# Kernel optimization log

Hardware: AMD Instinct MI355X
Metric: run time of the kernel (lower is better)

Reference implementation:

```python
import jax, jax.numpy as jnp
import numpy as np

# --- MLA config (DeepSeek-V3 style, scaled) ---
HIDDEN = 4096
N_HEADS = 32
Q_LORA = 1536
KV_LORA = 512
ROPE_D = 64
NOPE_D = 128
V_D = 128
Q_HEAD_D = NOPE_D + ROPE_D  # 192
EPS = 1e-6
SCALING = Q_HEAD_D ** (-0.5)
ROPE_THETA = 10000.0
B, S = 1, 2048


def rms_norm(x, w):
    var = jnp.mean(jnp.square(x.astype(jnp.float32)), axis=-1, keepdims=True)
    return (x * jax.lax.rsqrt(var + EPS)).astype(x.dtype) * w


def rotate_half(x):
    x1, x2 = jnp.split(x, 2, axis=-1)
    return jnp.concatenate([-x2, x1], axis=-1)


def apply_rope(x, cos, sin):
    # x: [B, H, S, ROPE_D]; cos/sin: [B, S, ROPE_D] -> unsqueeze head dim
    c = cos[:, None, :, :]
    s = sin[:, None, :, :]
    return x * c + rotate_half(x) * s


def setup_inputs() -> dict:
    key = jax.random.key(0)
    ks = jax.random.split(key, 8)
    hidden_states = jax.random.normal(ks[0], (B, S, HIDDEN), dtype=jnp.float32)
    # real RoPE tables
    inv_freq = 1.0 / (ROPE_THETA ** (np.arange(0, ROPE_D, 2, dtype=np.float32) / ROPE_D))
    t = np.arange(S, dtype=np.float32)
    freqs = np.outer(t, inv_freq)                      # [S, ROPE_D/2]
    emb = np.concatenate([freqs, freqs], axis=-1)      # [S, ROPE_D]
    cos = jnp.asarray(np.cos(emb))[None].repeat(B, 0)  # [B, S, ROPE_D]
    sin = jnp.asarray(np.sin(emb))[None].repeat(B, 0)
    scale = lambda fan_in: 1.0 / np.sqrt(fan_in)
    w_q_a = jax.random.normal(ks[1], (Q_LORA, HIDDEN), dtype=jnp.float32) * scale(HIDDEN)
    q_a_ln_w = jnp.ones((Q_LORA,), dtype=jnp.float32)
    w_q_b = jax.random.normal(ks[2], (N_HEADS * Q_HEAD_D, Q_LORA), dtype=jnp.float32) * scale(Q_LORA)
    w_kv_a = jax.random.normal(ks[3], (KV_LORA + ROPE_D, HIDDEN), dtype=jnp.float32) * scale(HIDDEN)
    kv_a_ln_w = jnp.ones((KV_LORA,), dtype=jnp.float32)
    w_kv_b = jax.random.normal(ks[4], (N_HEADS * (NOPE_D + V_D), KV_LORA), dtype=jnp.float32) * scale(KV_LORA)
    w_o = jax.random.normal(ks[5], (HIDDEN, N_HEADS * V_D), dtype=jnp.float32) * scale(N_HEADS * V_D)
    return {
        'hidden_states': hidden_states, 'cos': cos, 'sin': sin,
        'w_q_a': w_q_a, 'q_a_ln_w': q_a_ln_w, 'w_q_b': w_q_b,
        'w_kv_a': w_kv_a, 'kv_a_ln_w': kv_a_ln_w, 'w_kv_b': w_kv_b, 'w_o': w_o,
    }


def reference(hidden_states, cos, sin, w_q_a, q_a_ln_w, w_q_b, w_kv_a, kv_a_ln_w, w_kv_b, w_o):
    b, s, _ = hidden_states.shape
    # --- Q path: low-rank down + RMSNorm + up ---
    q_lat = rms_norm(hidden_states @ w_q_a.T, q_a_ln_w)              # [B,S,Q_LORA]
    q = (q_lat @ w_q_b.T).reshape(b, s, N_HEADS, Q_HEAD_D)
    q = q.transpose(0, 2, 1, 3)                                       # [B,H,S,Q_HEAD_D]
    q_nope, q_rot = q[..., :NOPE_D], q[..., NOPE_D:]                  # (note: source names swapped)
    # --- KV path: shared compressed latent + single rotary key ---
    ckv = hidden_states @ w_kv_a.T                                    # [B,S,KV_LORA+ROPE_D]
    k_lat, k_rot = ckv[..., :KV_LORA], ckv[..., KV_LORA:]
    kv = (rms_norm(k_lat, kv_a_ln_w) @ w_kv_b.T).reshape(b, s, N_HEADS, NOPE_D + V_D)
    kv = kv.transpose(0, 2, 1, 3)                                     # [B,H,S,NOPE_D+V_D]
    k_nope, v = kv[..., :NOPE_D], kv[..., NOPE_D:]
    k_rot = k_rot.reshape(b, 1, s, ROPE_D)                            # single rotary key head
    # --- partial RoPE on rotary slices ---
    q_rot = apply_rope(q_rot, cos, sin)
    k_rot = apply_rope(k_rot, cos, sin)
    k_rot = jnp.broadcast_to(k_rot, (b, N_HEADS, s, ROPE_D))
    query = jnp.concatenate([q_rot, q_nope], axis=-1)                 # [B,H,S,192]
    key = jnp.concatenate([k_rot, k_nope], axis=-1)                   # [B,H,S,192]
    # --- eager causal attention ---
    scores = jnp.einsum('bhqd,bhkd->bhqk', query, key) * SCALING
    causal = jnp.tril(jnp.ones((s, s), dtype=bool))
    scores = jnp.where(causal[None, None], scores, jnp.finfo(scores.dtype).min)
    probs = jax.nn.softmax(scores, axis=-1)
    attn = jnp.einsum('bhqk,bhkd->bhqd', probs, v)                    # [B,H,S,V_D]
    attn = attn.transpose(0, 2, 1, 3).reshape(b, s, N_HEADS * V_D)
    return attn @ w_o.T                                               # [B,S,HIDDEN]
```

## Files before the change

### kernel.cpp

```cpp
#include <hip/hip_runtime.h>

typedef unsigned short u16;
typedef u16 u16x4 __attribute__((ext_vector_type(4)));
typedef u16 u16x8 __attribute__((ext_vector_type(8)));
typedef float f32x4 __attribute__((ext_vector_type(4)));
typedef __bf16 bf16x8 __attribute__((ext_vector_type(8)));

#define S_LEN 2048
#define HIDDEN_D 4096
#define NHEADS 32
#define QLORA 1536
#define KVLORA 512
#define ROPED 64
#define NOPED 128
#define VDIM 128
#define QHD 192
#define SCALING_F 0.07216878364870323f

__device__ __forceinline__ u16 f2bf(float x) {
  union { float f; unsigned u; } v; v.f = x;
  unsigned r = v.u + 0x7fffu + ((v.u >> 16) & 1u);
  return (u16)(r >> 16);
}
__device__ __forceinline__ float bf2f(u16 x) {
  union { unsigned u; float f; } v; v.u = ((unsigned)x) << 16; return v.f;
}

__device__ __forceinline__ f32x4 mfma_bf16(u16x8 a, u16x8 b, f32x4 c) {
  return __builtin_amdgcn_mfma_f32_16x16x32_bf16(
      __builtin_bit_cast(bf16x8, a), __builtin_bit_cast(bf16x8, b), c, 0, 0, 0);
}

__global__ __launch_bounds__(256) void cvt_kernel(const float* __restrict__ in,
                                                  u16* __restrict__ out, int n4) {
  int i = blockIdx.x * 256 + threadIdx.x;
  if (i >= n4) return;
  f32x4 v = ((const f32x4*)in)[i];
  u16x4 o;
  o[0] = f2bf(v[0]); o[1] = f2bf(v[1]); o[2] = f2bf(v[2]); o[3] = f2bf(v[3]);
  ((u16x4*)out)[i] = o;
}


#define GEMM_PROLOGUE()                                                        \
  __shared__ u16 sA[2][128 * 64];                                              \
  __shared__ u16 sB[2][128 * 64];                                              \
  const int tid = threadIdx.x;                                                 \
  const int wid = tid >> 6, lane = tid & 63;                                   \
  const int lr = lane & 15, lg = lane >> 4;                                    \
  const int nbn = (N + 127) >> 7;                                              \
  const int bx = blockIdx.x % nbn, by = blockIdx.x / nbn;                      \
  const int bm = by << 7, bn = bx << 7;                                        \
  const int wm = (wid >> 1) << 6, wn = (wid & 1) << 6;                         \
  const int kbase = blockIdx.y * Ks;                                           \
  f32x4 acc[4][4] = {};                                                        \
  u16x8 areg[4], breg[4];                                                      \
  auto loadA = [&](int k0) {                                                   \
    _Pragma("unroll")                                                          \
    for (int i = 0; i < 4; ++i) {                                              \
      int chunk = i * 256 + tid;                                               \
      int row = chunk >> 3, c8 = chunk & 7;                                    \
      int gr = bm + row; if (gr >= M) gr = M - 1;                              \
      areg[i] = *(const u16x8*)(A + (size_t)gr * lda + k0 + (c8 << 3));        \
    }                                                                          \
  };                                                                           \
  auto loadB = [&](int k0) {                                                   \
    _Pragma("unroll")                                                          \
    for (int i = 0; i < 4; ++i) {                                              \
      int chunk = i * 256 + tid;                                               \
      int n = chunk >> 3, c8 = chunk & 7;                                      \
      int gn = bn + n; if (gn >= N) gn = N - 1;                                \
      breg[i] = *(const u16x8*)(B + (size_t)gn * ldb + k0 + (c8 << 3));        \
    }                                                                          \
  };                                                                           \
  auto writeAB = [&](int buf) {                                                \
    _Pragma("unroll")                                                          \
    for (int i = 0; i < 4; ++i) {                                              \
      *(u16x8*)&sA[buf][(i * 256 + tid) * 8] = areg[i];                        \
      *(u16x8*)&sB[buf][(i * 256 + tid) * 8] = breg[i];                        \
    }                                                                          \
  };                                                                           \
  auto compute = [&](int buf) {                                                \
    const u16* pa = sA[buf];                                                   \
    const u16* pb = sB[buf];                                                   \
    _Pragma("unroll")                                                          \
    for (int ks = 0; ks < 2; ++ks) {                                           \
      const int kof = ks * 32 + lg * 8;                                        \
      u16x8 av[4], bv[4];                                                      \
      _Pragma("unroll")                                                        \
      for (int m = 0; m < 4; ++m) av[m] = *(const u16x8*)&pa[(wm + m * 16 + lr) * 64 + kof]; \
      _Pragma("unroll")                                                        \
      for (int n = 0; n < 4; ++n) bv[n] = *(const u16x8*)&pb[(wn + n * 16 + lr) * 64 + kof]; \
      _Pragma("unroll")                                                        \
      for (int m = 0; m < 4; ++m)                                              \
        _Pragma("unroll")                                                      \
        for (int n = 0; n < 4; ++n)                                            \
          acc[m][n] = mfma_bf16(av[m], bv[n], acc[m][n]);                      \
    }                                                                          \
  };                                                                           \
  const int nk = Ks >> 6;                                                      \
  loadA(kbase); loadB(kbase);                                                  \
  writeAB(0);                                                                  \
  __syncthreads();                                                             \
  for (int t = 0; t < nk; ++t) {                                               \
    const int cur = t & 1;                                                     \
    if (t + 1 < nk) { loadA(kbase + ((t + 1) << 6)); loadB(kbase + ((t + 1) << 6)); } \
    compute(cur);                                                              \
    if (t + 1 < nk) { writeAB(cur ^ 1); }                                      \
    __syncthreads();                                                           \
  }

__global__ __launch_bounds__(256, 2) void gemm_ff(
    const u16* __restrict__ A, const u16* __restrict__ B, float* __restrict__ C,
    int M, int N, int Ks, int lda, int ldb, int ldc)
{
  C += (size_t)blockIdx.y * M * ldc;
  GEMM_PROLOGUE()
#pragma unroll
  for (int m = 0; m < 4; ++m) {
    const int row0 = bm + wm + m * 16 + (lg << 2);
#pragma unroll
    for (int n = 0; n < 4; ++n) {
      const int col = bn + wn + n * 16 + lr;
      if (col < N) {
#pragma unroll
        for (int r = 0; r < 4; ++r)
          C[(size_t)(row0 + r) * ldc + col] = acc[m][n][r];
      }
    }
  }
}

__global__ __launch_bounds__(256, 2) void gemm_fb(
    const u16* __restrict__ A, const u16* __restrict__ B, u16* __restrict__ C,
    int M, int N, int Ks, int lda, int ldb, int ldc)
{
  GEMM_PROLOGUE()
#pragma unroll
  for (int m = 0; m < 4; ++m) {
    const int row0 = bm + wm + m * 16 + (lg << 2);
#pragma unroll
    for (int n = 0; n < 4; ++n) {
      const int col = bn + wn + n * 16 + lr;
#pragma unroll
      for (int r = 0; r < 4; ++r)
        C[(size_t)(row0 + r) * ldc + col] = f2bf(acc[m][n][r]);
    }
  }
}

__global__ __launch_bounds__(256, 2) void gemm_kvb(
    const u16* __restrict__ A, const u16* __restrict__ B,
    u16* __restrict__ Knope, u16* __restrict__ Vt,
    int M, int N, int Ks, int lda, int ldb)
{
  GEMM_PROLOGUE()
#pragma unroll
  for (int m = 0; m < 4; ++m) {
    const int row0 = bm + wm + m * 16 + (lg << 2);
#pragma unroll
    for (int n = 0; n < 4; ++n) {
      const int col = bn + wn + n * 16 + lr;
      const int h = col >> 8, c = col & 255;
      if (c < 128) {
#pragma unroll
        for (int r = 0; r < 4; ++r)
          Knope[((size_t)h * 2048 + row0 + r) * 128 + c] = f2bf(acc[m][n][r]);
      } else {
        u16x4 v;
        v[0] = f2bf(acc[m][n][0]); v[1] = f2bf(acc[m][n][1]);
        v[2] = f2bf(acc[m][n][2]); v[3] = f2bf(acc[m][n][3]);
        *(u16x4*)&Vt[((size_t)h * 128 + (c - 128)) * 2048 + row0] = v;
      }
    }
  }
}

__global__ __launch_bounds__(256) void rms_kernel(const float* __restrict__ X,
                                                  const float* __restrict__ w,
                                                  u16* __restrict__ out, int D,
                                                  int nparts, size_t pstride) {
  const int row = blockIdx.x;
  const float* x = X + (size_t)row * D;
  __shared__ float sb[4];
  float ss = 0.f;
  for (int i = threadIdx.x * 4; i < D; i += 1024) {
    f32x4 v = *(const f32x4*)&x[i];
    for (int pp = 1; pp < nparts; ++pp) {
      f32x4 v2 = *(const f32x4*)&x[pp * pstride + i];
      v[0] += v2[0]; v[1] += v2[1]; v[2] += v2[2]; v[3] += v2[3];
    }
    ss += v[0] * v[0] + v[1] * v[1] + v[2] * v[2] + v[3] * v[3];
  }
#pragma unroll
  for (int off = 32; off >= 1; off >>= 1) ss += __shfl_xor(ss, off, 64);
  if ((threadIdx.x & 63) == 0) sb[threadIdx.x >> 6] = ss;
  __syncthreads();
  const float inv = rsqrtf((sb[0] + sb[1] + sb[2] + sb[3]) / (float)D + 1e-6f);
  u16* o = out + (size_t)row * D;
  for (int i = threadIdx.x * 4; i < D; i += 1024) {
    f32x4 v = *(const f32x4*)&x[i];
    for (int pp = 1; pp < nparts; ++pp) {
      f32x4 v2 = *(const f32x4*)&x[pp * pstride + i];
      v[0] += v2[0]; v[1] += v2[1]; v[2] += v2[2]; v[3] += v2[3];
    }
    f32x4 wv = *(const f32x4*)&w[i];
    u16x4 u;
    u[0] = f2bf(v[0] * inv * wv[0]); u[1] = f2bf(v[1] * inv * wv[1]);
    u[2] = f2bf(v[2] * inv * wv[2]); u[3] = f2bf(v[3] * inv * wv[3]);
    *(u16x4*)&o[i] = u;
  }
}

__global__ __launch_bounds__(256) void ckv_epi_kernel(const float* __restrict__ ckv,
    const float* __restrict__ w, const float* __restrict__ cosp, const float* __restrict__ sinp,
    u16* __restrict__ klatn, u16* __restrict__ krot, int nparts, size_t pstride) {
  const int s = blockIdx.x;
  const float* x = ckv + (size_t)s * 576;
  __shared__ float sb[4];
  const int i2 = threadIdx.x * 2;
  float a = 0.f, b = 0.f;
  for (int pp = 0; pp < nparts; ++pp) {
    a += x[pp * pstride + i2];
    b += x[pp * pstride + i2 + 1];
  }
  float ss = a * a + b * b;
#pragma unroll
  for (int off = 32; off >= 1; off >>= 1) ss += __shfl_xor(ss, off, 64);
  if ((threadIdx.x & 63) == 0) sb[threadIdx.x >> 6] = ss;
  __syncthreads();
  const float inv = rsqrtf((sb[0] + sb[1] + sb[2] + sb[3]) / 512.0f + 1e-6f);
  klatn[(size_t)s * 512 + i2]     = f2bf(a * inv * w[i2]);
  klatn[(size_t)s * 512 + i2 + 1] = f2bf(b * inv * w[i2 + 1]);
  if (threadIdx.x < 64) {
    const int d = threadIdx.x;
    float xr = 0.f, rrabs = 0.f;
    for (int pp = 0; pp < nparts; ++pp) {
      xr += x[pp * pstride + 512 + d];
      rrabs += x[pp * pstride + 512 + ((d < 32) ? (d + 32) : (d - 32))];
    }
    const float rr = (d < 32) ? -rrabs : rrabs;
    krot[(size_t)s * 64 + d] = f2bf(xr * cosp[s * 64 + d] + rr * sinp[s * 64 + d]);
  }
}

__global__ __launch_bounds__(256) void q_epi_kernel(const u16* __restrict__ q_raw,
    const float* __restrict__ cosp, const float* __restrict__ sinp, u16* __restrict__ Qb) {
  const int s = blockIdx.x;
  const u16* x = q_raw + (size_t)s * 6144;
  for (int idx = threadIdx.x; idx < 6144; idx += 256) {
    const int h = idx / 192, d = idx - h * 192;
    float v;
    if (d < 64) {
      const float xr = bf2f(x[h * 192 + 128 + d]);
      const float rr = (d < 32) ? -bf2f(x[h * 192 + 160 + d]) : bf2f(x[h * 192 + 96 + d]);
      v = xr * cosp[s * 64 + d] + rr * sinp[s * 64 + d];
    } else {
      v = bf2f(x[h * 192 + d - 64]);
    }
    Qb[((size_t)h * 2048 + s) * QHD + d] = f2bf(v * SCALING_F);
  }
}

__global__ __launch_bounds__(256, 2) void flash_kernel(
    const u16* __restrict__ Qb, const u16* __restrict__ Krot,
    const u16* __restrict__ Knope, const u16* __restrict__ Vt,
    u16* __restrict__ attnb)
{
  const int h = blockIdx.x & 31, qt = blockIdx.x >> 5;
  const int q0 = qt << 7;
  __shared__ u16 sK[64][QHD];
  __shared__ u16 sV[VDIM][64];
  __shared__ u16 sP[4][32][64];
  const int tid = threadIdx.x;
  const int wid = tid >> 6, lane = tid & 63;
  const int lr = lane & 15, lg = lane >> 4;

  u16x8 qf[2][6];
#pragma unroll
  for (int m = 0; m < 2; ++m) {
    const int row = q0 + wid * 32 + m * 16 + lr;
#pragma unroll
    for (int kk = 0; kk < 6; ++kk)
      qf[m][kk] = *(const u16x8*)&Qb[((size_t)h * 2048 + row) * QHD + kk * 32 + lg * 8];
  }

  f32x4 acc[2][8] = {};
  float mx[2][4], ls[2][4];
#pragma unroll
  for (int m = 0; m < 2; ++m)
#pragma unroll
    for (int r = 0; r < 4; ++r) { mx[m][r] = -1e30f; ls[m][r] = 0.f; }

  const int nkv = q0 + 128;
  u16x8 kreg[6], vreg[4];

  auto loadKV = [&](int kv0) {
#pragma unroll
    for (int i = 0; i < 6; ++i) {
      const int chunk = i * 256 + tid;
      const int row = chunk / 24, cc = chunk % 24;
      const u16* src = (cc < 8)
          ? &Krot[(size_t)(kv0 + row) * 64 + cc * 8]
          : &Knope[((size_t)h * 2048 + kv0 + row) * 128 + (cc - 8) * 8];
      kreg[i] = *(const u16x8*)src;
    }
#pragma unroll
    for (int i = 0; i < 4; ++i) {
      const int chunk = i * 256 + tid;
      const int d = chunk >> 3, c = chunk & 7;
      vreg[i] = *(const u16x8*)&Vt[((size_t)h * VDIM + d) * 2048 + kv0 + c * 8];
    }
  };

  loadKV(0);
  for (int kv0 = 0; kv0 < nkv; kv0 += 64) {
    __syncthreads();
    u16* kbase = &sK[0][0];
#pragma unroll
    for (int i = 0; i < 6; ++i) *(u16x8*)&kbase[(size_t)(i * 256 + tid) * 8] = kreg[i];
    u16* vbase = &sV[0][0];
#pragma unroll
    for (int i = 0; i < 4; ++i) *(u16x8*)&vbase[(size_t)(i * 256 + tid) * 8] = vreg[i];
    __syncthreads();
    if (kv0 + 64 < nkv) loadKV(kv0 + 64);

    f32x4 sc[2][4] = {};
#pragma unroll
    for (int kk = 0; kk < 6; ++kk) {
      u16x8 bfr[4];
#pragma unroll
      for (int n = 0; n < 4; ++n) bfr[n] = *(const u16x8*)&sK[n * 16 + lr][kk * 32 + lg * 8];
#pragma unroll
      for (int m = 0; m < 2; ++m)
#pragma unroll
        for (int n = 0; n < 4; ++n)
          sc[m][n] = mfma_bf16(qf[m][kk], bfr[n], sc[m][n]);
    }

    if (kv0 + 63 > q0 + wid * 32) {
#pragma unroll
      for (int m = 0; m < 2; ++m)
#pragma unroll
        for (int n = 0; n < 4; ++n) {
          const int kv = kv0 + n * 16 + lr;
#pragma unroll
          for (int r = 0; r < 4; ++r) {
            const int rowq = q0 + wid * 32 + m * 16 + lg * 4 + r;
            if (kv > rowq) sc[m][n][r] = -1e30f;
          }
        }
    }

#pragma unroll
    for (int m = 0; m < 2; ++m) {
      float rs[4];
#pragma unroll
      for (int r = 0; r < 4; ++r) {
        float v = fmaxf(fmaxf(sc[m][0][r], sc[m][1][r]), fmaxf(sc[m][2][r], sc[m][3][r]));
#pragma unroll
        for (int off = 1; off < 16; off <<= 1) v = fmaxf(v, __shfl_xor(v, off, 64));
        const float mnew = fmaxf(mx[m][r], v);
        const float alpha = __expf(mx[m][r] - mnew);
        mx[m][r] = mnew;
        ls[m][r] *= alpha;
#pragma unroll
        for (int df = 0; df < 8; ++df) acc[m][df][r] *= alpha;
        rs[r] = 0.f;
      }
#pragma unroll
      for (int n = 0; n < 4; ++n)
#pragma unroll
        for (int r = 0; r < 4; ++r) {
          const float p = __expf(sc[m][n][r] - mx[m][r]);
          rs[r] += p;
          sP[wid][m * 16 + lg * 4 + r][n * 16 + lr] = f2bf(p);
        }
#pragma unroll
      for (int r = 0; r < 4; ++r) {
        float v = rs[r];
#pragma unroll
        for (int off = 1; off < 16; off <<= 1) v += __shfl_xor(v, off, 64);
        ls[m][r] += v;
      }
    }

#pragma unroll
    for (int ks = 0; ks < 2; ++ks) {
      u16x8 pf0 = *(const u16x8*)&sP[wid][lr][ks * 32 + lg * 8];
      u16x8 pf1 = *(const u16x8*)&sP[wid][16 + lr][ks * 32 + lg * 8];
#pragma unroll
      for (int df = 0; df < 8; ++df) {
        u16x8 vf = *(const u16x8*)&sV[df * 16 + lr][ks * 32 + lg * 8];
        acc[0][df] = mfma_bf16(pf0, vf, acc[0][df]);
        acc[1][df] = mfma_bf16(pf1, vf, acc[1][df]);
      }
    }
  }

#pragma unroll
  for (int m = 0; m < 2; ++m)
#pragma unroll
    for (int df = 0; df < 8; ++df) {
      const int col = h * 128 + df * 16 + lr;
#pragma unroll
      for (int r = 0; r < 4; ++r) {
        const int row = q0 + wid * 32 + m * 16 + lg * 4 + r;
        attnb[(size_t)row * 4096 + col] = f2bf(acc[m][df][r] / ls[m][r]);
      }
    }
}

extern "C" void kernel_launch(void* const* d_in, const int* in_sizes, int n_in,
                              void* d_out, int out_size, void* d_ws, size_t ws_size,
                              hipStream_t stream) {
  (void)in_sizes; (void)n_in; (void)out_size; (void)ws_size;
  const float* hidden  = (const float*)d_in[0];
  const float* cosp    = (const float*)d_in[1];
  const float* sinp    = (const float*)d_in[2];
  const float* w_q_a   = (const float*)d_in[3];
  const float* q_a_ln  = (const float*)d_in[4];
  const float* w_q_b   = (const float*)d_in[5];
  const float* w_kv_a  = (const float*)d_in[6];
  const float* kv_a_ln = (const float*)d_in[7];
  const float* w_kv_b  = (const float*)d_in[8];
  const float* w_o     = (const float*)d_in[9];
  float* out = (float*)d_out;

  char* p = (char*)d_ws;
  auto alloc = [&](size_t bytes) { char* r = p; p += (bytes + 255) & ~(size_t)255; return r; };
  u16* Hb     = (u16*)alloc((size_t)S_LEN * HIDDEN_D * 2);
  u16* qlatn  = (u16*)alloc((size_t)S_LEN * QLORA * 2);
  u16* klatn  = (u16*)alloc((size_t)S_LEN * KVLORA * 2);
  u16* krot   = (u16*)alloc((size_t)S_LEN * ROPED * 2);
  u16* Qb     = (u16*)alloc((size_t)NHEADS * S_LEN * QHD * 2);
  u16* Knope  = (u16*)alloc((size_t)NHEADS * S_LEN * NOPED * 2);
  u16* Vt     = (u16*)alloc((size_t)NHEADS * VDIM * S_LEN * 2);
  u16* attnb  = (u16*)alloc((size_t)S_LEN * 4096 * 2);
  u16* Wqa    = (u16*)alloc((size_t)QLORA * HIDDEN_D * 2);
  u16* Wqb    = (u16*)alloc((size_t)6144 * QLORA * 2);
  u16* Wkva   = (u16*)alloc((size_t)576 * HIDDEN_D * 2);
  u16* Wkvb   = (u16*)alloc((size_t)8192 * KVLORA * 2);
  u16* Wo     = (u16*)alloc((size_t)HIDDEN_D * 4096 * 2);
  u16* qraw16 = (u16*)alloc((size_t)S_LEN * 6144 * 2);
  float* qa_part  = (float*)alloc((size_t)2 * S_LEN * QLORA * 4);
  float* kva_part = (float*)alloc((size_t)4 * S_LEN * 576 * 4);

  cvt_kernel<<<(S_LEN * HIDDEN_D / 4 + 255) / 256, 256, 0, stream>>>(hidden, Hb, S_LEN * HIDDEN_D / 4);
  cvt_kernel<<<(QLORA * HIDDEN_D / 4 + 255) / 256, 256, 0, stream>>>(w_q_a, Wqa, QLORA * HIDDEN_D / 4);
  cvt_kernel<<<(6144 * QLORA / 4 + 255) / 256, 256, 0, stream>>>(w_q_b, Wqb, 6144 * QLORA / 4);
  cvt_kernel<<<(576 * HIDDEN_D / 4 + 255) / 256, 256, 0, stream>>>(w_kv_a, Wkva, 576 * HIDDEN_D / 4);
  cvt_kernel<<<(8192 * KVLORA / 4 + 255) / 256, 256, 0, stream>>>(w_kv_b, Wkvb, 8192 * KVLORA / 4);
  cvt_kernel<<<(HIDDEN_D * 4096 / 4 + 255) / 256, 256, 0, stream>>>(w_o, Wo, HIDDEN_D * 4096 / 4);

  gemm_ff<<<dim3(16 * 12, 2), 256, 0, stream>>>(Hb, Wqa, qa_part, 2048, 1536, 2048, 4096, 4096, 1536);
  gemm_ff<<<dim3(16 * 5, 4), 256, 0, stream>>>(Hb, Wkva, kva_part, 2048, 576, 1024, 4096, 4096, 576);
  rms_kernel<<<2048, 256, 0, stream>>>(qa_part, q_a_ln, qlatn, 1536, 2, (size_t)S_LEN * QLORA);
  ckv_epi_kernel<<<2048, 256, 0, stream>>>(kva_part, kv_a_ln, cosp, sinp, klatn, krot, 4, (size_t)S_LEN * 576);
  gemm_fb<<<dim3(16 * 48, 1), 256, 0, stream>>>(qlatn, Wqb, qraw16, 2048, 6144, 1536, 1536, 1536, 6144);
  q_epi_kernel<<<2048, 256, 0, stream>>>(qraw16, cosp, sinp, Qb);
  gemm_kvb<<<dim3(16 * 64, 1), 256, 0, stream>>>(klatn, Wkvb, Knope, Vt, 2048, 8192, 512, 512, 512);
  flash_kernel<<<512, 256, 0, stream>>>(Qb, krot, Knope, Vt, attnb);
  gemm_ff<<<dim3(16 * 32, 1), 256, 0, stream>>>(attnb, Wo, out, 2048, 4096, 4096, 4096, 4096, 4096);
}
```

Baseline: 604.7 us.

## Load GEMM tiles directly global-to-LDS with single buffer

The shared GEMM mainloop now uses global_load_lds so tile data goes straight from global memory into LDS, with no staging through registers. It drops the double-buffered register-prefetch pipeline in favour of a single LDS buffer with two barriers per k-step, and relaxes the launch bounds' minimum-blocks hint. This frees VGPRs and removes the LDS write instructions, but global loads no longer overlap with MFMA compute inside a block, so latency hiding depends on other resident blocks. Using the 16-byte width of the builtin assumes hardware support for it.

```diff
diff --git a/kernel.cpp b/kernel.cpp
--- a/kernel.cpp
+++ b/kernel.cpp
@@ -17,6 +17,9 @@
 #define QHD 192
 #define SCALING_F 0.07216878364870323f
 
+#define GLOBAL_U32 const __attribute__((address_space(1))) unsigned int
+#define LDS_U32 __attribute__((address_space(3))) unsigned int
+
 __device__ __forceinline__ u16 f2bf(float x) {
   union { float f; unsigned u; } v; v.f = x;
   unsigned r = v.u + 0x7fffu + ((v.u >> 16) & 1u);
@@ -43,8 +46,8 @@
 
 
 #define GEMM_PROLOGUE()                                                        \
-  __shared__ u16 sA[2][128 * 64];                                              \
-  __shared__ u16 sB[2][128 * 64];                                              \
+  __shared__ u16 sA[128 * 64];                                                 \
+  __shared__ u16 sB[128 * 64];                                                 \
   const int tid = threadIdx.x;                                                 \
   const int wid = tid >> 6, lane = tid & 63;                                   \
   const int lr = lane & 15, lg = lane >> 4;                                    \
@@ -54,63 +57,44 @@
   const int wm = (wid >> 1) << 6, wn = (wid & 1) << 6;                         \
   const int kbase = blockIdx.y * Ks;                                           \
   f32x4 acc[4][4] = {};                                                        \
-  u16x8 areg[4], breg[4];                                                      \
-  auto loadA = [&](int k0) {                                                   \
+  const int nk = Ks >> 6;                                                      \
+  for (int t = 0; t < nk; ++t) {                                               \
+    const int k0 = kbase + (t << 6);                                           \
     _Pragma("unroll")                                                          \
     for (int i = 0; i < 4; ++i) {                                              \
       int chunk = i * 256 + tid;                                               \
       int row = chunk >> 3, c8 = chunk & 7;                                    \
       int gr = bm + row; if (gr >= M) gr = M - 1;                              \
-      areg[i] = *(const u16x8*)(A + (size_t)gr * lda + k0 + (c8 << 3));        \
+      const u16* gp = A + (size_t)gr * lda + k0 + (c8 << 3);                   \
+      __builtin_amdgcn_global_load_lds((GLOBAL_U32*)gp, (LDS_U32*)&sA[chunk * 8], 16, 0, 0); \
     }                                                                          \
-  };                                                                           \
-  auto loadB = [&](int k0) {                                                   \
     _Pragma("unroll")                                                          \
     for (int i = 0; i < 4; ++i) {                                              \
       int chunk = i * 256 + tid;                                               \
-      int n = chunk >> 3, c8 = chunk & 7;                                      \
-      int gn = bn + n; if (gn >= N) gn = N - 1;                                \
-      breg[i] = *(const u16x8*)(B + (size_t)gn * ldb + k0 + (c8 << 3));        \
+      int row = chunk >> 3, c8 = chunk & 7;                                    \
+      int gn = bn + row; if (gn >= N) gn = N - 1;                              \
+      const u16* gp = B + (size_t)gn * ldb + k0 + (c8 << 3);                   \
+      __builtin_amdgcn_global_load_lds((GLOBAL_U32*)gp, (LDS_U32*)&sB[chunk * 8], 16, 0, 0); \
     }                                                                          \
-  };                                                                           \
-  auto writeAB = [&](int buf) {                                                \
-    _Pragma("unroll")                                                          \
-    for (int i = 0; i < 4; ++i) {                                              \
-      *(u16x8*)&sA[buf][(i * 256 + tid) * 8] = areg[i];                        \
-      *(u16x8*)&sB[buf][(i * 256 + tid) * 8] = breg[i];                        \
-    }                                                                          \
-  };                                                                           \
-  auto compute = [&](int buf) {                                                \
-    const u16* pa = sA[buf];                                                   \
-    const u16* pb = sB[buf];                                                   \
+    __syncthreads();                                                           \
     _Pragma("unroll")                                                          \
     for (int ks = 0; ks < 2; ++ks) {                                           \
       const int kof = ks * 32 + lg * 8;                                        \
       u16x8 av[4], bv[4];                                                      \
       _Pragma("unroll")                                                        \
-      for (int m = 0; m < 4; ++m) av[m] = *(const u16x8*)&pa[(wm + m * 16 + lr) * 64 + kof]; \
+      for (int m = 0; m < 4; ++m) av[m] = *(const u16x8*)&sA[(wm + m * 16 + lr) * 64 + kof]; \
       _Pragma("unroll")                                                        \
-      for (int n = 0; n < 4; ++n) bv[n] = *(const u16x8*)&pb[(wn + n * 16 + lr) * 64 + kof]; \
+      for (int n = 0; n < 4; ++n) bv[n] = *(const u16x8*)&sB[(wn + n * 16 + lr) * 64 + kof]; \
       _Pragma("unroll")                                                        \
       for (int m = 0; m < 4; ++m)                                              \
         _Pragma("unroll")                                                      \
         for (int n = 0; n < 4; ++n)                                            \
           acc[m][n] = mfma_bf16(av[m], bv[n], acc[m][n]);                      \
     }                                                                          \
-  };                                                                           \
-  const int nk = Ks >> 6;                                                      \
-  loadA(kbase); loadB(kbase);                                                  \
-  writeAB(0);                                                                  \
-  __syncthreads();                                                             \
-  for (int t = 0; t < nk; ++t) {                                               \
-    const int cur = t & 1;                                                     \
-    if (t + 1 < nk) { loadA(kbase + ((t + 1) << 6)); loadB(kbase + ((t + 1) << 6)); } \
-    compute(cur);                                                              \
-    if (t + 1 < nk) { writeAB(cur ^ 1); }                                      \
     __syncthreads();                                                           \
   }
 
-__global__ __launch_bounds__(256, 2) void gemm_ff(
+__global__ __launch_bounds__(256) void gemm_ff(
     const u16* __restrict__ A, const u16* __restrict__ B, float* __restrict__ C,
     int M, int N, int Ks, int lda, int ldb, int ldc)
 {
@@ -131,7 +115,7 @@
   }
 }
 
-__global__ __launch_bounds__(256, 2) void gemm_fb(
+__global__ __launch_bounds__(256) void gemm_fb(
     const u16* __restrict__ A, const u16* __restrict__ B, u16* __restrict__ C,
     int M, int N, int Ks, int lda, int ldb, int ldc)
 {
@@ -149,7 +133,7 @@
   }
 }
 
-__global__ __launch_bounds__(256, 2) void gemm_kvb(
+__global__ __launch_bounds__(256) void gemm_kvb(
     const u16* __restrict__ A, const u16* __restrict__ B,
     u16* __restrict__ Knope, u16* __restrict__ Vt,
     int M, int N, int Ks, int lda, int ldb)
```

New measurement: 637.2 us. 1.05x slower.
